# Performance work log

Measured on AMD Instinct MI355X. Metric: run time of the kernel, lower is better.

Reference implementation:

```python
import jax, jax.numpy as jnp
import numpy as np

OUT_SIZE = (224, 224)  # (Ho, Wo)


def setup_inputs() -> dict:
    key = jax.random.key(0)
    k1, k2, k3 = jax.random.split(key, 3)
    B, H, W_in, C = 16, 224, 224, 32
    F = 128
    x = jax.random.normal(k1, (B, H, W_in, C), dtype=jnp.float32)
    theta_feat = jax.random.normal(k2, (B, F), dtype=jnp.float32)
    # localisation head params: W small (original inits zeros), b = flattened 2x3 identity
    W = jax.random.normal(k3, (F, 6), dtype=jnp.float32) * 0.01
    b = jnp.array([1.0, 0.0, 0.0, 0.0, 1.0, 0.0], dtype=jnp.float32)
    return {"x": x, "theta_feat": theta_feat, "W": W, "b": b}


def _transform(im, theta, out_size):
    # im: [B,H,W,C], theta: [B,6] -> affine grid sample, border-clamped bilinear
    B, H, W_in, C = im.shape
    Ho, Wo = out_size
    Hf = jnp.float32(H)
    Wf = jnp.float32(W_in)

    # normalized target grid in [-1, 1], homogeneous coords [3, N]
    x_t = jnp.linspace(-1.0, 1.0, Wo, dtype=jnp.float32)
    y_t = jnp.linspace(-1.0, 1.0, Ho, dtype=jnp.float32)
    xg, yg = jnp.meshgrid(x_t, y_t)  # [Ho, Wo]
    grid = jnp.stack([xg.ravel(), yg.ravel(), jnp.ones(Ho * Wo, jnp.float32)])  # [3, N]

    T = theta.reshape(B, 2, 3)
    src = jnp.einsum('bij,jn->bin', T, grid)  # [B, 2, N]
    xs = src[:, 0, :]  # [B, N] in [-1,1]
    ys = src[:, 1, :]

    # map to source pixel coords (original transformer uses width/2, not (width-1)/2)
    xp = (xs + 1.0) * Wf / 2.0
    yp = (ys + 1.0) * Hf / 2.0

    x0 = jnp.floor(xp).astype(jnp.int32)
    x1 = x0 + 1
    y0 = jnp.floor(yp).astype(jnp.int32)
    y1 = y0 + 1
    x0 = jnp.clip(x0, 0, W_in - 1)
    x1 = jnp.clip(x1, 0, W_in - 1)
    y0 = jnp.clip(y0, 0, H - 1)
    y1 = jnp.clip(y1, 0, H - 1)

    x0f = x0.astype(jnp.float32)
    x1f = x1.astype(jnp.float32)
    y0f = y0.astype(jnp.float32)
    y1f = y1.astype(jnp.float32)
    wa = (x1f - xp) * (y1f - yp)
    wb = (x1f - xp) * (yp - y0f)
    wc = (xp - x0f) * (y1f - yp)
    wd = (xp - x0f) * (yp - y0f)

    im_flat = im.reshape(B, H * W_in, C)

    def gather(yy, xx):
        idx = (yy * W_in + xx)[..., None]  # [B, N, 1]
        return jnp.take_along_axis(im_flat, idx, axis=1)  # [B, N, C]

    Ia = gather(y0, x0)
    Ib = gather(y1, x0)
    Ic = gather(y0, x1)
    Id = gather(y1, x1)

    out = (wa[..., None] * Ia + wb[..., None] * Ib
           + wc[..., None] * Ic + wd[..., None] * Id)  # [B, N, C]
    return out.reshape(B, Ho, Wo, C)


def reference(x, theta_feat, W, b):
    theta = jnp.tanh(theta_feat @ W + b)  # [B, 6]
    return _transform(x, theta, OUT_SIZE)
```

## Files before the change

kernel.cpp:

```cpp
#include <hip/hip_runtime.h>
#include <math.h>

#define BATCH 16
#define HIN   224
#define WIN   224
#define CCH   32
#define FDIM  128
#define HOUT  224
#define WOUT  224

#define PIX_PER_BATCH (HOUT * WOUT)
#define BLOCK 256
#define ITEMS_PER_THREAD 2
#define ITEMS_PER_BLOCK (BLOCK * ITEMS_PER_THREAD)
#define PIX_PER_BLOCK (ITEMS_PER_BLOCK / 8)
#define BLOCKS_PER_BATCH (PIX_PER_BATCH / PIX_PER_BLOCK)
#define NBLOCKS (BATCH * BLOCKS_PER_BATCH)
#define NXCD 8
#define BLOCKS_PER_XCD (NBLOCKS / NXCD)

__global__ void st_theta_kernel(const float* __restrict__ tf,
                                const float* __restrict__ Wm,
                                const float* __restrict__ bv,
                                float* __restrict__ theta) {
    int wid  = (int)((blockIdx.x * blockDim.x + threadIdx.x) >> 6);
    int lane = (int)(threadIdx.x & 63);
    if (wid >= BATCH * 6) return;
    int bi = wid / 6;
    int j  = wid - bi * 6;
    const float* row = tf + bi * FDIM;
    float acc = row[lane] * Wm[lane * 6 + j]
              + row[lane + 64] * Wm[(lane + 64) * 6 + j];
    acc += __shfl_xor(acc, 32);
    acc += __shfl_xor(acc, 16);
    acc += __shfl_xor(acc, 8);
    acc += __shfl_xor(acc, 4);
    acc += __shfl_xor(acc, 2);
    acc += __shfl_xor(acc, 1);
    if (lane == 0) theta[wid] = tanhf(acc + bv[j]);
}

__global__ __launch_bounds__(BLOCK) void st_sample_kernel(
        const float* __restrict__ im,
        const float* __restrict__ theta,
        float* __restrict__ out) {

    int bid = blockIdx.x;
    int nb  = (bid & (NXCD - 1)) * BLOCKS_PER_XCD + (bid >> 3);

    int b = nb / BLOCKS_PER_BATCH;

    const float* th = theta + b * 6;
    float t0 = th[0], t1 = th[1], t2 = th[2];
    float t3 = th[3], t4 = th[4], t5 = th[5];

    const float4* imf4 = (const float4*)im;
    float4* of4 = (float4*)out;
    size_t ibase = (size_t)b * (size_t)(HIN * WIN * 8);

    int base = nb * ITEMS_PER_BLOCK + (int)threadIdx.x;

    size_t addr[ITEMS_PER_THREAD][4];
    float  wgt[ITEMS_PER_THREAD][4];
    int    oidx[ITEMS_PER_THREAD];

#pragma unroll
    for (int u = 0; u < ITEMS_PER_THREAD; ++u) {
        int i  = base + u * BLOCK;
        int p  = i >> 3;
        int c4 = i & 7;

        int rem = p - b * PIX_PER_BATCH;
        int ho  = rem / WOUT;
        int wo  = rem - ho * WOUT;

        float x_t = -1.0f + (2.0f * (float)wo) / (float)(WOUT - 1);
        float y_t = -1.0f + (2.0f * (float)ho) / (float)(HOUT - 1);

        float xs = t0 * x_t + t1 * y_t + t2;
        float ys = t3 * x_t + t4 * y_t + t5;

        float xp = (xs + 1.0f) * (0.5f * (float)WIN);
        float yp = (ys + 1.0f) * (0.5f * (float)HIN);

        int x0 = (int)floorf(xp);
        int y0 = (int)floorf(yp);
        int x1 = x0 + 1;
        int y1 = y0 + 1;

        x0 = min(max(x0, 0), WIN - 1);
        x1 = min(max(x1, 0), WIN - 1);
        y0 = min(max(y0, 0), HIN - 1);
        y1 = min(max(y1, 0), HIN - 1);

        float x0f = (float)x0, x1f = (float)x1;
        float y0f = (float)y0, y1f = (float)y1;

        wgt[u][0] = (x1f - xp) * (y1f - yp);
        wgt[u][1] = (x1f - xp) * (yp - y0f);
        wgt[u][2] = (xp - x0f) * (y1f - yp);
        wgt[u][3] = (xp - x0f) * (yp - y0f);

        addr[u][0] = ibase + ((size_t)(y0 * WIN + x0)) * 8 + c4;
        addr[u][1] = ibase + ((size_t)(y1 * WIN + x0)) * 8 + c4;
        addr[u][2] = ibase + ((size_t)(y0 * WIN + x1)) * 8 + c4;
        addr[u][3] = ibase + ((size_t)(y1 * WIN + x1)) * 8 + c4;
        oidx[u] = i;
    }

    float4 v[ITEMS_PER_THREAD][4];
#pragma unroll
    for (int u = 0; u < ITEMS_PER_THREAD; ++u) {
#pragma unroll
        for (int t = 0; t < 4; ++t) {
            v[u][t] = imf4[addr[u][t]];
        }
    }

#pragma unroll
    for (int u = 0; u < ITEMS_PER_THREAD; ++u) {
        float4 o;
        o.x = wgt[u][0] * v[u][0].x + wgt[u][1] * v[u][1].x
            + wgt[u][2] * v[u][2].x + wgt[u][3] * v[u][3].x;
        o.y = wgt[u][0] * v[u][0].y + wgt[u][1] * v[u][1].y
            + wgt[u][2] * v[u][2].y + wgt[u][3] * v[u][3].y;
        o.z = wgt[u][0] * v[u][0].z + wgt[u][1] * v[u][1].z
            + wgt[u][2] * v[u][2].z + wgt[u][3] * v[u][3].z;
        o.w = wgt[u][0] * v[u][0].w + wgt[u][1] * v[u][1].w
            + wgt[u][2] * v[u][2].w + wgt[u][3] * v[u][3].w;
        of4[oidx[u]] = o;
    }
}

extern "C" void kernel_launch(void* const* d_in, const int* in_sizes, int n_in,
                              void* d_out, int out_size, void* d_ws, size_t ws_size,
                              hipStream_t stream) {
    const float* x  = (const float*)d_in[0];
    const float* tf = (const float*)d_in[1];
    const float* Wm = (const float*)d_in[2];
    const float* bv = (const float*)d_in[3];
    float* out = (float*)d_out;

    float* theta = (float*)d_ws;

    st_theta_kernel<<<24, 256, 0, stream>>>(tf, Wm, bv, theta);
    st_sample_kernel<<<NBLOCKS, BLOCK, 0, stream>>>(x, theta, out);
}
```

Measured before the change: 33.83 us.

## Double items per thread, use 32-bit gather offsets and nontemporal output stores

Raises items per thread from 2 to 4, which halves the block count and puts more gathers in flight per thread. Image offsets are computed in 32-bit unsigned instead of size_t, which reduces 64-bit address arithmetic and register use. Output is written with nontemporal stores so the streamed output does not evict the input from cache. The larger per-thread register footprint may lower occupancy.

```diff
diff --git a/kernel.cpp b/kernel.cpp
--- a/kernel.cpp
+++ b/kernel.cpp
@@ -11,13 +11,15 @@
 
 #define PIX_PER_BATCH (HOUT * WOUT)
 #define BLOCK 256
-#define ITEMS_PER_THREAD 2
+#define ITEMS_PER_THREAD 4
 #define ITEMS_PER_BLOCK (BLOCK * ITEMS_PER_THREAD)
 #define PIX_PER_BLOCK (ITEMS_PER_BLOCK / 8)
 #define BLOCKS_PER_BATCH (PIX_PER_BATCH / PIX_PER_BLOCK)
 #define NBLOCKS (BATCH * BLOCKS_PER_BATCH)
 #define NXCD 8
 #define BLOCKS_PER_XCD (NBLOCKS / NXCD)
+
+typedef float f32x4 __attribute__((ext_vector_type(4)));
 
 __global__ void st_theta_kernel(const float* __restrict__ tf,
                                 const float* __restrict__ Wm,
@@ -54,15 +56,14 @@
     float t0 = th[0], t1 = th[1], t2 = th[2];
     float t3 = th[3], t4 = th[4], t5 = th[5];
 
-    const float4* imf4 = (const float4*)im;
-    float4* of4 = (float4*)out;
-    size_t ibase = (size_t)b * (size_t)(HIN * WIN * 8);
+    const f32x4* imf4 = (const f32x4*)im;
+    f32x4* of4 = (f32x4*)out;
+    unsigned ibase = (unsigned)b * (unsigned)(HIN * WIN * 8);
 
     int base = nb * ITEMS_PER_BLOCK + (int)threadIdx.x;
 
-    size_t addr[ITEMS_PER_THREAD][4];
-    float  wgt[ITEMS_PER_THREAD][4];
-    int    oidx[ITEMS_PER_THREAD];
+    unsigned addr[ITEMS_PER_THREAD][4];
+    float    wgt[ITEMS_PER_THREAD][4];
 
 #pragma unroll
     for (int u = 0; u < ITEMS_PER_THREAD; ++u) {
@@ -101,14 +102,13 @@
         wgt[u][2] = (xp - x0f) * (y1f - yp);
         wgt[u][3] = (xp - x0f) * (yp - y0f);
 
-        addr[u][0] = ibase + ((size_t)(y0 * WIN + x0)) * 8 + c4;
-        addr[u][1] = ibase + ((size_t)(y1 * WIN + x0)) * 8 + c4;
-        addr[u][2] = ibase + ((size_t)(y0 * WIN + x1)) * 8 + c4;
-        addr[u][3] = ibase + ((size_t)(y1 * WIN + x1)) * 8 + c4;
-        oidx[u] = i;
+        addr[u][0] = ibase + (unsigned)(y0 * WIN + x0) * 8u + (unsigned)c4;
+        addr[u][1] = ibase + (unsigned)(y1 * WIN + x0) * 8u + (unsigned)c4;
+        addr[u][2] = ibase + (unsigned)(y0 * WIN + x1) * 8u + (unsigned)c4;
+        addr[u][3] = ibase + (unsigned)(y1 * WIN + x1) * 8u + (unsigned)c4;
     }
 
-    float4 v[ITEMS_PER_THREAD][4];
+    f32x4 v[ITEMS_PER_THREAD][4];
 #pragma unroll
     for (int u = 0; u < ITEMS_PER_THREAD; ++u) {
 #pragma unroll
@@ -119,16 +119,9 @@
 
 #pragma unroll
     for (int u = 0; u < ITEMS_PER_THREAD; ++u) {
-        float4 o;
-        o.x = wgt[u][0] * v[u][0].x + wgt[u][1] * v[u][1].x
-            + wgt[u][2] * v[u][2].x + wgt[u][3] * v[u][3].x;
-        o.y = wgt[u][0] * v[u][0].y + wgt[u][1] * v[u][1].y
-            + wgt[u][2] * v[u][2].y + wgt[u][3] * v[u][3].y;
-        o.z = wgt[u][0] * v[u][0].z + wgt[u][1] * v[u][1].z
-            + wgt[u][2] * v[u][2].z + wgt[u][3] * v[u][3].z;
-        o.w = wgt[u][0] * v[u][0].w + wgt[u][1] * v[u][1].w
-            + wgt[u][2] * v[u][2].w + wgt[u][3] * v[u][3].w;
-        of4[oidx[u]] = o;
+        f32x4 o = wgt[u][0] * v[u][0] + wgt[u][1] * v[u][1]
+                + wgt[u][2] * v[u][2] + wgt[u][3] * v[u][3];
+        __builtin_nontemporal_store(o, &of4[base + u * BLOCK]);
     }
 }
 
```

New measurement: 33.34 us. Within noise of the previous version (-1.5%).
